# Kernel optimization log

Measured on AMD Instinct MI355X. Metric: run time of the kernel, lower is better.

Reference implementation:

```python
import jax, jax.numpy as jnp
import numpy as np

B, T, C, H = 8, 2048, 1024, 64

def setup_inputs() -> dict:
    key = jax.random.key(0)
    kx, kq, kk, kv = jax.random.split(key, 4)
    scale = 1.0 / np.sqrt(C)
    return {
        "x": jax.random.normal(kx, (B, T, C), dtype=jnp.float32),
        "Wq": jax.random.normal(kq, (C, H), dtype=jnp.float32) * scale,
        "Wk": jax.random.normal(kk, (C, H), dtype=jnp.float32) * scale,
        "Wv": jax.random.normal(kv, (C, H), dtype=jnp.float32) * scale,
    }

def reference(x, Wq, Wk, Wv):
    # q,k,v: [B,T,H]
    q = jnp.einsum('btc,ch->bth', x, Wq)
    k = jnp.einsum('btc,ch->bth', x, Wk)
    v = jnp.einsum('btc,ch->bth', x, Wv)
    scale = k.shape[-1] ** -0.5
    wei = jnp.einsum('bth,bsh->bts', q, k) * scale  # [B,T,T]
    causal = jnp.tril(jnp.ones((x.shape[1], x.shape[1]), dtype=bool))
    wei = jnp.where(causal, wei, -jnp.inf)
    wei = jax.nn.softmax(wei, axis=-1)
    out = jnp.einsum('bts,bsh->bth', wei, v)  # [B,T,H]
    return out
```

## Files before the change

kernel.cpp:

```cpp
#include <hip/hip_runtime.h>

#define B_ 8
#define T_ 2048
#define C_ 1024
#define H_ 64

typedef __bf16 bf16x8 __attribute__((ext_vector_type(8)));
typedef float  f32x4  __attribute__((ext_vector_type(4)));
typedef unsigned short u16x8 __attribute__((ext_vector_type(8)));
typedef float  f32x4v __attribute__((ext_vector_type(4)));

__device__ __forceinline__ unsigned short f2bf(float f) {
    unsigned u = __builtin_bit_cast(unsigned, f);
    u += 0x8000u;
    return (unsigned short)(u >> 16);
}

__device__ __forceinline__ float bf2f(unsigned short v) {
    unsigned u = ((unsigned)v) << 16;
    return __builtin_bit_cast(float, u);
}

__device__ __forceinline__ unsigned pack2(float lo, float hi) {
    unsigned a = __builtin_bit_cast(unsigned, lo) + 0x8000u;
    unsigned b = __builtin_bit_cast(unsigned, hi) + 0x8000u;
    return (a >> 16) | (b & 0xffff0000u);
}

union U8 { unsigned u32[4]; u16x8 v; };

__device__ __forceinline__ u16x8 cvt8v(f32x4v f0, f32x4v f1) {
    U8 r;
    r.u32[0] = pack2(f0.x, f0.y);
    r.u32[1] = pack2(f0.z, f0.w);
    r.u32[2] = pack2(f1.x, f1.y);
    r.u32[3] = pack2(f1.z, f1.w);
    return r.v;
}

__device__ __forceinline__ bf16x8 load8_bf(const unsigned short* p) {
    return __builtin_bit_cast(bf16x8, *(const u16x8*)p);
}


__global__ void cast_weights(const float* __restrict__ Wq,
                             const float* __restrict__ Wk,
                             const float* __restrict__ Wv,
                             unsigned short* __restrict__ Wtf) {
    int idx = blockIdx.x * blockDim.x + threadIdx.x;
    int n   = idx % 192;
    int c   = idx / 192;
    int w   = n >> 6;
    int h   = n & 63;
    const float* W = (w == 0) ? Wq : (w == 1) ? Wk : Wv;
    int nt = n >> 4, l16 = n & 15;
    int kk = c >> 5, quad = (c >> 3) & 3, j = c & 7;
    Wtf[(size_t)(nt * 32 + kk) * 512 + l16 * 32 + quad * 8 + j] =
        f2bf(W[(size_t)c * H_ + h]);
}

__global__ __launch_bounds__(256) void qkv_proj(
        const float* __restrict__ x,
        const unsigned short* __restrict__ Wtf,
        unsigned short* __restrict__ Qf,
        unsigned short* __restrict__ Kf,
        unsigned short* __restrict__ Vf) {
    __shared__ __attribute__((aligned(16))) unsigned short As_[32 * 512];

    const int tid  = threadIdx.x;
    const int ns   = tid >> 6;
    const int lane = tid & 63;
    const int l16  = lane & 15;
    const int quad = lane >> 4;
    const size_t r0 = (size_t)blockIdx.x * 32;
    const int bb    = (int)(r0 >> 11);
    const int tloc0 = (int)(r0 & (T_ - 1));
    const int t16_0 = tloc0 >> 4;
    const int s32   = tloc0 >> 5;

    f32x4 acc[6];
#pragma unroll
    for (int i = 0; i < 6; i++) acc[i] = (f32x4){0.f, 0.f, 0.f, 0.f};

    const int sw   = l16 & 7;
    const int loff = l16 * 32 + quad * 8;

    for (int p = 0; p < 2; p++) {
        if (p) __syncthreads();
#pragma unroll
        for (int i = 0; i < 8; i++) {
            int c   = i * 256 + tid;
            int row = c >> 6;
            int g   = c & 63;
            const float* sp = x + (r0 + row) * C_ + p * 512 + g * 8;
            f32x4v f0 = __builtin_nontemporal_load((const f32x4v*)sp);
            f32x4v f1 = __builtin_nontemporal_load((const f32x4v*)(sp + 4));
            int off = row * 512 + ((g & ~7) + ((g & 7) ^ (row & 7))) * 8;
            *(u16x8*)(&As_[off]) = cvt8v(f0, f1);
        }
        __syncthreads();

#pragma unroll 4
        for (int kc = 0; kc < 16; kc++) {
            int g  = kc * 4 + quad;
            int gs = ((g & ~7) + ((g & 7) ^ sw)) * 8;
            bf16x8 a0 = load8_bf(&As_[l16 * 512 + gs]);
            bf16x8 a1 = load8_bf(&As_[(16 + l16) * 512 + gs]);
            int kk = p * 16 + kc;
#pragma unroll
            for (int i = 0; i < 3; i++) {
                bf16x8 b = load8_bf(Wtf + (size_t)((ns * 3 + i) * 32 + kk) * 512 + loff);
                acc[i]     = __builtin_amdgcn_mfma_f32_16x16x32_bf16(a0, b, acc[i],     0, 0, 0);
                acc[3 + i] = __builtin_amdgcn_mfma_f32_16x16x32_bf16(a1, b, acc[3 + i], 0, 0, 0);
            }
        }
    }

    __syncthreads();
    unsigned short* E = As_;
#pragma unroll
    for (int i = 0; i < 3; i++) {
        int nt = ns * 3 + i;
#pragma unroll
        for (int msI = 0; msI < 2; msI++) {
#pragma unroll
            for (int r = 0; r < 4; r++) {
                unsigned short bv = f2bf(acc[msI * 3 + i][r]);
                int off;
                int ch;
                if (nt < 4) {
                    ch  = msI * 2 + (nt >> 1);
                    off = (quad * 4 + r) * 32 + ((nt & 1) * 2 + (l16 >> 3)) * 8 + (l16 & 7);
                } else if (nt < 8) {
                    int nk = nt - 4;
                    ch  = 4 + msI * 2 + (nk >> 1);
                    off = (quad * 4 + r) * 32 + ((nk & 1) * 2 + (l16 >> 3)) * 8 + (l16 & 7);
                } else {
                    int w32 = msI * 16 + quad * 4 + r;
                    ch  = 8 + (nt - 8);
                    off = l16 * 32 + (w32 >> 3) * 8 + (w32 & 7);
                }
                E[ch * 512 + off] = bv;
            }
        }
    }
    __syncthreads();

#pragma unroll
    for (int i = 0; i < 3; i++) {
        int gi = i * 256 + tid;
        int ch = gi >> 6;
        int g  = gi & 63;
        unsigned short* dst;
        if (ch < 4) {
            dst = Qf + ((size_t)(bb * 128 + t16_0 + (ch >> 1)) * 2 + (ch & 1)) * 512;
        } else if (ch < 8) {
            int c2 = ch - 4;
            dst = Kf + ((size_t)(bb * 128 + t16_0 + (c2 >> 1)) * 2 + (c2 & 1)) * 512;
        } else {
            dst = Vf + ((size_t)(bb * 64 + s32) * 4 + (ch - 8)) * 512;
        }
        __builtin_nontemporal_store(*(const u16x8*)(&E[ch * 512 + g * 8]),
                                    (u16x8*)(dst + g * 8));
    }
}

#define PROW 33
#define OMS2 66

__global__ __launch_bounds__(256) void attn(
        const unsigned short* __restrict__ Qf,
        const unsigned short* __restrict__ Kf,
        const unsigned short* __restrict__ Vf,
        float* __restrict__ out) {
    __shared__ unsigned int ps_[4 * 32 * PROW];
    __shared__ unsigned short Om_[4 * 32 * OMS2];
    __shared__ float mred_[4][32];
    __shared__ float lred_[4][32];

    const int tid  = threadIdx.x;
    const int wave = tid >> 6;
    const int lane = tid & 63;
    const int l16  = lane & 15;
    const int quad = lane >> 4;
    const int b    = blockIdx.x & 7;
    const int qt32 = blockIdx.x >> 3;
    const int q0   = qt32 * 32;
    const int tdiag = qt32 >> 1;

    const int loff = l16 * 32 + quad * 8;

    bf16x8 qf[2][2];
#pragma unroll
    for (int qg = 0; qg < 2; qg++) {
        const unsigned short* Qfb = Qf + (size_t)((b * 128 + qt32 * 2 + qg) * 2) * 512;
        qf[qg][0] = load8_bf(Qfb + loff);
        qf[qg][1] = load8_bf(Qfb + 512 + loff);
    }

    f32x4 o[8];
#pragma unroll
    for (int i = 0; i < 8; i++) o[i] = (f32x4){0.f, 0.f, 0.f, 0.f};
    float m_run[2] = {-1e30f, -1e30f}, l_run[2] = {0.f, 0.f};

    const float scale = 0.125f;
    const unsigned short* Kfb = Kf + (size_t)b * 128 * 1024;
    const unsigned short* Vfb = Vf + (size_t)b * 64 * 2048;
    unsigned int* Pw = &ps_[wave * 32 * PROW];

    for (int t = wave; t <= tdiag; t += 4) {
        bf16x8 vf[8];
#pragma unroll
        for (int ks = 0; ks < 2; ks++)
#pragma unroll
            for (int ht = 0; ht < 4; ht++)
                vf[ht * 2 + ks] = load8_bf(
                    Vfb + ((size_t)(t * 2 + ks) * 4 + ht) * 512 + loff);

        f32x4 s[2][4];
#pragma unroll
        for (int nt = 0; nt < 4; nt++) {
            const unsigned short* kp = Kfb + (size_t)(t * 4 + nt) * 1024;
            bf16x8 kf0 = load8_bf(kp + loff);
            bf16x8 kf1 = load8_bf(kp + 512 + loff);
#pragma unroll
            for (int qg = 0; qg < 2; qg++) {
                f32x4 z = (f32x4){0.f, 0.f, 0.f, 0.f};
                z = __builtin_amdgcn_mfma_f32_16x16x32_bf16(kf0, qf[qg][0], z, 0, 0, 0);
                z = __builtin_amdgcn_mfma_f32_16x16x32_bf16(kf1, qf[qg][1], z, 0, 0, 0);
                s[qg][nt] = z;
            }
        }

#pragma unroll
        for (int qg = 0; qg < 2; qg++)
#pragma unroll
            for (int nt = 0; nt < 4; nt++)
#pragma unroll
                for (int r = 0; r < 4; r++) s[qg][nt][r] *= scale;

        if (t == tdiag) {
#pragma unroll
            for (int qg = 0; qg < 2; qg++) {
                int q = q0 + qg * 16 + l16;
#pragma unroll
                for (int nt = 0; nt < 4; nt++)
#pragma unroll
                    for (int r = 0; r < 4; r++) {
                        int key = t * 64 + nt * 16 + quad * 4 + r;
                        if (key > q) s[qg][nt][r] = -1e30f;
                    }
            }
        }

#pragma unroll
        for (int qg = 0; qg < 2; qg++) {
            float m0 = fmaxf(fmaxf(s[qg][0][0], s[qg][0][1]), fmaxf(s[qg][0][2], s[qg][0][3]));
            float m1 = fmaxf(fmaxf(s[qg][1][0], s[qg][1][1]), fmaxf(s[qg][1][2], s[qg][1][3]));
            float m2 = fmaxf(fmaxf(s[qg][2][0], s[qg][2][1]), fmaxf(s[qg][2][2], s[qg][2][3]));
            float m3 = fmaxf(fmaxf(s[qg][3][0], s[qg][3][1]), fmaxf(s[qg][3][2], s[qg][3][3]));
            float mx = fmaxf(fmaxf(m0, m1), fmaxf(m2, m3));
            mx = fmaxf(mx, __shfl_xor(mx, 16));
            mx = fmaxf(mx, __shfl_xor(mx, 32));
            const float m_new = fmaxf(m_run[qg], mx);
            const float alpha = __expf(m_run[qg] - m_new);
            m_run[qg] = m_new;

            float rs = 0.f;
#pragma unroll
            for (int nt = 0; nt < 4; nt++) {
#pragma unroll
                for (int i = 0; i < 2; i++) {
                    float p0 = __expf(s[qg][nt][2 * i]     - m_new);
                    float p1 = __expf(s[qg][nt][2 * i + 1] - m_new);
                    rs += p0 + p1;
                    Pw[(qg * 16 + l16) * PROW + nt * 8 + quad * 2 + i] = pack2(p0, p1);
                }
            }
            rs += __shfl_xor(rs, 16);
            rs += __shfl_xor(rs, 32);
            l_run[qg] = l_run[qg] * alpha + rs;

#pragma unroll
            for (int ht = 0; ht < 4; ht++)
#pragma unroll
                for (int r = 0; r < 4; r++) o[qg * 4 + ht][r] *= alpha;
        }

#pragma unroll
        for (int ks = 0; ks < 2; ks++) {
#pragma unroll
            for (int qg = 0; qg < 2; qg++) {
                bf16x8 pB = __builtin_bit_cast(bf16x8,
                    *(const u16x8*)(&Pw[(qg * 16 + l16) * PROW + ks * 16 + quad * 4]));
#pragma unroll
                for (int ht = 0; ht < 4; ht++)
                    o[qg * 4 + ht] = __builtin_amdgcn_mfma_f32_16x16x32_bf16(
                        vf[ht * 2 + ks], pB, o[qg * 4 + ht], 0, 0, 0);
            }
        }
    }

#pragma unroll
    for (int qg = 0; qg < 2; qg++) {
#pragma unroll
        for (int ht = 0; ht < 4; ht++)
#pragma unroll
            for (int r = 0; r < 4; r++)
                Om_[(wave * 32 + qg * 16 + l16) * OMS2 + ht * 16 + quad * 4 + r] =
                    f2bf(o[qg * 4 + ht][r]);
        if (quad == 0) {
            mred_[wave][qg * 16 + l16] = m_run[qg];
            lred_[wave][qg * 16 + l16] = l_run[qg];
        }
    }
    __syncthreads();

    const int hcol = tid & 63;
    const int qr0  = tid >> 6;
#pragma unroll
    for (int qq = 0; qq < 8; qq++) {
        const int q = qr0 + qq * 4;
        float M = -1e30f;
#pragma unroll
        for (int w = 0; w < 4; w++) M = fmaxf(M, mred_[w][q]);
        float lt = 0.f, ov = 0.f;
#pragma unroll
        for (int w = 0; w < 4; w++) {
            float e = __expf(mred_[w][q] - M);
            lt += e * lred_[w][q];
            ov += e * bf2f(Om_[(w * 32 + q) * OMS2 + hcol]);
        }
        out[((size_t)b * T_ + q0 + q) * H_ + hcol] = ov / lt;
    }
}

extern "C" void kernel_launch(void* const* d_in, const int* in_sizes, int n_in,
                              void* d_out, int out_size, void* d_ws, size_t ws_size,
                              hipStream_t stream) {
    const float* x  = (const float*)d_in[0];
    const float* Wq = (const float*)d_in[1];
    const float* Wk = (const float*)d_in[2];
    const float* Wv = (const float*)d_in[3];
    float* out = (float*)d_out;

    unsigned short* Qf  = (unsigned short*)d_ws;
    unsigned short* Kf  = Qf + (size_t)B_ * T_ * H_;
    unsigned short* Vf  = Kf + (size_t)B_ * T_ * H_;
    unsigned short* Wtf = Vf + (size_t)B_ * T_ * H_;

    cast_weights<<<(192 * C_) / 256, 256, 0, stream>>>(Wq, Wk, Wv, Wtf);
    qkv_proj<<<B_ * T_ / 32, 256, 0, stream>>>(x, Wtf, Qf, Kf, Vf);
    attn<<<B_ * (T_ / 32), 256, 0, stream>>>(Qf, Kf, Vf, out);
}
```

Measured before the change: 153.9 us.

## Retile QKV projection to 128-row blocks with double-buffered K-loop prefetch

The projection kernel now processes 128 rows per block with 8 waves. Each wave computes 32 rows by 96 output columns, so weight fragments are reused across more rows. The K dimension is walked in 16 steps of 64, and the next x chunk is prefetched into registers and written to a second LDS buffer while MFMAs run on the current one. This is meant to hide global load latency and cut redundant weight reads. In exchange it uses more registers, launches fewer blocks, and drops the nontemporal hints.

```diff
diff --git a/kernel.cpp b/kernel.cpp
--- a/kernel.cpp
+++ b/kernel.cpp
@@ -59,85 +59,111 @@
         f2bf(W[(size_t)c * H_ + h]);
 }
 
-__global__ __launch_bounds__(256) void qkv_proj(
+__global__ __launch_bounds__(512) void qkv_proj(
         const float* __restrict__ x,
         const unsigned short* __restrict__ Wtf,
         unsigned short* __restrict__ Qf,
         unsigned short* __restrict__ Kf,
         unsigned short* __restrict__ Vf) {
-    __shared__ __attribute__((aligned(16))) unsigned short As_[32 * 512];
+    __shared__ __attribute__((aligned(16))) unsigned short As_[24576];
 
     const int tid  = threadIdx.x;
-    const int ns   = tid >> 6;
+    const int wave = tid >> 6;
     const int lane = tid & 63;
     const int l16  = lane & 15;
     const int quad = lane >> 4;
-    const size_t r0 = (size_t)blockIdx.x * 32;
+    const int mp   = wave >> 1;
+    const int nh   = wave & 1;
+    const size_t r0 = (size_t)blockIdx.x * 128;
     const int bb    = (int)(r0 >> 11);
     const int tloc0 = (int)(r0 & (T_ - 1));
     const int t16_0 = tloc0 >> 4;
-    const int s32   = tloc0 >> 5;
-
-    f32x4 acc[6];
-#pragma unroll
-    for (int i = 0; i < 6; i++) acc[i] = (f32x4){0.f, 0.f, 0.f, 0.f};
-
-    const int sw   = l16 & 7;
+    const int s32_0 = tloc0 >> 5;
+
+    f32x4 acc[2][6];
+#pragma unroll
+    for (int st = 0; st < 2; st++)
+#pragma unroll
+        for (int i = 0; i < 6; i++) acc[st][i] = (f32x4){0.f, 0.f, 0.f, 0.f};
+
     const int loff = l16 * 32 + quad * 8;
-
-    for (int p = 0; p < 2; p++) {
-        if (p) __syncthreads();
-#pragma unroll
-        for (int i = 0; i < 8; i++) {
-            int c   = i * 256 + tid;
-            int row = c >> 6;
-            int g   = c & 63;
-            const float* sp = x + (r0 + row) * C_ + p * 512 + g * 8;
-            f32x4v f0 = __builtin_nontemporal_load((const f32x4v*)sp);
-            f32x4v f1 = __builtin_nontemporal_load((const f32x4v*)(sp + 4));
-            int off = row * 512 + ((g & ~7) + ((g & 7) ^ (row & 7))) * 8;
-            *(u16x8*)(&As_[off]) = cvt8v(f0, f1);
-        }
-        __syncthreads();
-
-#pragma unroll 4
-        for (int kc = 0; kc < 16; kc++) {
-            int g  = kc * 4 + quad;
-            int gs = ((g & ~7) + ((g & 7) ^ sw)) * 8;
-            bf16x8 a0 = load8_bf(&As_[l16 * 512 + gs]);
-            bf16x8 a1 = load8_bf(&As_[(16 + l16) * 512 + gs]);
-            int kk = p * 16 + kc;
-#pragma unroll
-            for (int i = 0; i < 3; i++) {
-                bf16x8 b = load8_bf(Wtf + (size_t)((ns * 3 + i) * 32 + kk) * 512 + loff);
-                acc[i]     = __builtin_amdgcn_mfma_f32_16x16x32_bf16(a0, b, acc[i],     0, 0, 0);
-                acc[3 + i] = __builtin_amdgcn_mfma_f32_16x16x32_bf16(a1, b, acc[3 + i], 0, 0, 0);
-            }
-        }
-    }
-
+    const unsigned short* wb = Wtf + (size_t)(nh * 6) * 32 * 512;
+
+    const int row0 = tid >> 3, g0 = tid & 7;
+    const int row1 = (tid + 512) >> 3, g1 = tid & 7;
+    const float* src0 = x + (r0 + row0) * C_ + g0 * 8;
+    const float* src1 = x + (r0 + row1) * C_ + g1 * 8;
+    const int off0 = row0 * 64 + ((g0 ^ (row0 & 7)) * 8);
+    const int off1 = row1 * 64 + ((g1 ^ (row1 & 7)) * 8);
+
+    {
+        f32x4v a0 = *(const f32x4v*)src0;
+        f32x4v a1 = *(const f32x4v*)(src0 + 4);
+        f32x4v b0 = *(const f32x4v*)src1;
+        f32x4v b1 = *(const f32x4v*)(src1 + 4);
+        *(u16x8*)(&As_[off0]) = cvt8v(a0, a1);
+        *(u16x8*)(&As_[off1]) = cvt8v(b0, b1);
+    }
     __syncthreads();
-    unsigned short* E = As_;
-#pragma unroll
-    for (int i = 0; i < 3; i++) {
-        int nt = ns * 3 + i;
-#pragma unroll
-        for (int msI = 0; msI < 2; msI++) {
+
+    int cur = 0;
+    for (int ks = 0; ks < 16; ks++) {
+        const bool more = (ks < 15);
+        f32x4v n00, n01, n10, n11;
+        if (more) {
+            const float* s0 = src0 + (ks + 1) * 64;
+            const float* s1 = src1 + (ks + 1) * 64;
+            n00 = *(const f32x4v*)s0;
+            n01 = *(const f32x4v*)(s0 + 4);
+            n10 = *(const f32x4v*)s1;
+            n11 = *(const f32x4v*)(s1 + 4);
+        }
+        const unsigned short* Ac = As_ + cur * 8192;
+#pragma unroll
+        for (int kk = 0; kk < 2; kk++) {
+            bf16x8 a[2];
+#pragma unroll
+            for (int st = 0; st < 2; st++) {
+                int arow = (mp * 2 + st) * 16 + l16;
+                a[st] = load8_bf(&Ac[arow * 64 + (((kk * 4 + quad) ^ (arow & 7)) * 8)]);
+            }
+#pragma unroll
+            for (int i = 0; i < 6; i++) {
+                bf16x8 b = load8_bf(wb + (size_t)(i * 32 + ks * 2 + kk) * 512 + loff);
+                acc[0][i] = __builtin_amdgcn_mfma_f32_16x16x32_bf16(a[0], b, acc[0][i], 0, 0, 0);
+                acc[1][i] = __builtin_amdgcn_mfma_f32_16x16x32_bf16(a[1], b, acc[1][i], 0, 0, 0);
+            }
+        }
+        if (more) {
+            const int nxt = cur ^ 1;
+            *(u16x8*)(&As_[nxt * 8192 + off0]) = cvt8v(n00, n01);
+            *(u16x8*)(&As_[nxt * 8192 + off1]) = cvt8v(n10, n11);
+            __syncthreads();
+            cur = nxt;
+        }
+    }
+
+    __syncthreads();
+    unsigned short* E = &As_[wave * 3072];
+#pragma unroll
+    for (int i = 0; i < 6; i++) {
+        int nt = nh * 6 + i;
+#pragma unroll
+        for (int st = 0; st < 2; st++) {
 #pragma unroll
             for (int r = 0; r < 4; r++) {
-                unsigned short bv = f2bf(acc[msI * 3 + i][r]);
-                int off;
-                int ch;
+                unsigned short bv = f2bf(acc[st][i][r]);
+                int ch, off;
                 if (nt < 4) {
-                    ch  = msI * 2 + (nt >> 1);
+                    ch  = st * 3 + (nt >> 1);
                     off = (quad * 4 + r) * 32 + ((nt & 1) * 2 + (l16 >> 3)) * 8 + (l16 & 7);
                 } else if (nt < 8) {
                     int nk = nt - 4;
-                    ch  = 4 + msI * 2 + (nk >> 1);
+                    ch  = (nh == 0) ? (st * 3 + 2) : st;
                     off = (quad * 4 + r) * 32 + ((nk & 1) * 2 + (l16 >> 3)) * 8 + (l16 & 7);
                 } else {
-                    int w32 = msI * 16 + quad * 4 + r;
-                    ch  = 8 + (nt - 8);
+                    int w32 = st * 16 + quad * 4 + r;
+                    ch  = 2 + (nt - 8);
                     off = l16 * 32 + (w32 >> 3) * 8 + (w32 & 7);
                 }
                 E[ch * 512 + off] = bv;
@@ -147,21 +173,24 @@
     __syncthreads();
 
 #pragma unroll
-    for (int i = 0; i < 3; i++) {
-        int gi = i * 256 + tid;
-        int ch = gi >> 6;
-        int g  = gi & 63;
+    for (int c = 0; c < 6; c++) {
         unsigned short* dst;
-        if (ch < 4) {
-            dst = Qf + ((size_t)(bb * 128 + t16_0 + (ch >> 1)) * 2 + (ch & 1)) * 512;
-        } else if (ch < 8) {
-            int c2 = ch - 4;
-            dst = Kf + ((size_t)(bb * 128 + t16_0 + (c2 >> 1)) * 2 + (c2 & 1)) * 512;
+        if (nh == 0) {
+            int st = (c < 3) ? 0 : 1;
+            int j  = c - st * 3;
+            int t16 = t16_0 + mp * 2 + st;
+            if (j < 2) dst = Qf + ((size_t)(bb * 128 + t16) * 2 + j) * 512;
+            else       dst = Kf + ((size_t)(bb * 128 + t16) * 2 + 0) * 512;
         } else {
-            dst = Vf + ((size_t)(bb * 64 + s32) * 4 + (ch - 8)) * 512;
-        }
-        __builtin_nontemporal_store(*(const u16x8*)(&E[ch * 512 + g * 8]),
-                                    (u16x8*)(dst + g * 8));
+            if (c < 2) {
+                int t16 = t16_0 + mp * 2 + c;
+                dst = Kf + ((size_t)(bb * 128 + t16) * 2 + 1) * 512;
+            } else {
+                int s32 = s32_0 + mp;
+                dst = Vf + ((size_t)(bb * 64 + s32) * 4 + (c - 2)) * 512;
+            }
+        }
+        *(u16x8*)(dst + lane * 8) = *(const u16x8*)(&E[c * 512 + lane * 8]);
     }
 }
 
@@ -350,6 +379,6 @@
     unsigned short* Wtf = Vf + (size_t)B_ * T_ * H_;
 
     cast_weights<<<(192 * C_) / 256, 256, 0, stream>>>(Wq, Wk, Wv, Wtf);
-    qkv_proj<<<B_ * T_ / 32, 256, 0, stream>>>(x, Wtf, Qf, Kf, Vf);
+    qkv_proj<<<B_ * T_ / 128, 512, 0, stream>>>(x, Wtf, Qf, Kf, Vf);
     attn<<<B_ * (T_ / 32), 256, 0, stream>>>(Qf, Kf, Vf, out);
 }
```

Result: slower. 167.8 us (+9.0%).
